# Kernel tuning notes

Hardware: AMD Instinct MI355X
Metric: run time of the kernel (lower is better)

The kernel has to match this reference:

```python
import jax, jax.numpy as jnp
import numpy as np
import math


def setup_inputs() -> dict:
    key = jax.random.key(0)
    ks = jax.random.split(key, 4)
    B, C, H, W, D = 16, 512, 64, 64, 256
    return {
        "x": jax.random.normal(ks[0], (B, C, H, W), jnp.float32),
        "weight_global": jax.random.normal(ks[1], (C, D), jnp.float32) * 0.02,  # trunc_normal std=0.02
        "conv_g_w": jax.random.normal(ks[2], (C, C), jnp.float32) * 0.02,       # 1x1 conv, no bias
        "bn_g_gamma": jnp.ones((C,), jnp.float32),
        "bn_g_beta": jnp.zeros((C,), jnp.float32),
        "conv_c_w": jax.random.normal(ks[3], (C, C), jnp.float32) * 0.02,
        "bn_c_gamma": jnp.ones((C,), jnp.float32),
        "bn_c_beta": jnp.zeros((C,), jnp.float32),
    }


def _bn(x, gamma, beta, eps=1e-5):
    # BatchNorm2d in default training mode: batch statistics over (B, H, W)
    mean = x.mean(axis=(0, 2, 3), keepdims=True)
    var = x.var(axis=(0, 2, 3), keepdims=True)
    xn = (x - mean) * jax.lax.rsqrt(var + eps)
    return xn * gamma[None, :, None, None] + beta[None, :, None, None]


def reference(x, weight_global, conv_g_w, bn_g_gamma, bn_g_beta, conv_c_w, bn_c_gamma, bn_c_beta):
    b, c, h, w = x.shape
    inv_sqrt_c = 1.0 / math.sqrt(c)

    # Description: QR-orthogonal codebook, Q: (c, d)
    Q, _ = jnp.linalg.qr(weight_global + 1e-8)

    # global branch: 1x1 conv -> BN -> ReLU -> global avg pool
    gx = jnp.einsum('oc,bchw->bohw', conv_g_w, x)
    gx = jax.nn.relu(_bn(gx, bn_g_gamma, bn_g_beta))
    g = gx.mean(axis=(2, 3))                                  # (b, c)
    aff_g = jax.nn.softmax((g @ Q) * inv_sqrt_c, axis=1)      # (b, d)
    g = jax.nn.sigmoid(aff_g @ Q.T)                           # (b, c)

    # channel branch: 1x1 conv -> BN -> ReLU
    cx = jnp.einsum('oc,bchw->bohw', conv_c_w, x)
    cx = jax.nn.relu(_bn(cx, bn_c_gamma, bn_c_beta))
    ch = cx.reshape(b, c, h * w).transpose(0, 2, 1)           # (b, hw, c)
    aff_c = jax.nn.softmax((ch @ Q) * inv_sqrt_c, axis=2)     # (b, hw, d)
    # sum(diag_embed(aff_c) @ Q.T, dim=2) == aff_c @ Q.T (fused, avoids (b,hw,d,c) intermediate)
    ch = aff_c @ Q.T                                          # (b, hw, c)

    o = ch * g[:, None, :]
    o = o.transpose(0, 2, 1).reshape(b, c, h, w)
    return o + x
```

## Files before the change

kernel.cpp:

```cpp
#include <hip/hip_runtime.h>
#include <hip/hip_bf16.h>

#define BB 16
#define CC 512
#define HWP 4096
#define DD 256
#define NPIX 65536
#define INV_SQRT_C 0.04419417382415922f

typedef unsigned short u16;
typedef __attribute__((ext_vector_type(8))) short s16x8;
typedef __attribute__((ext_vector_type(8))) unsigned short u16x8;
typedef __attribute__((ext_vector_type(4))) unsigned short u16x4;
typedef __attribute__((ext_vector_type(4))) float f32x4;

__device__ __forceinline__ u16 f2b(float f){
  unsigned int u = __builtin_bit_cast(unsigned int, f);
  unsigned int r = (u + 0x7fffu + ((u >> 16) & 1u)) >> 16;
  return (u16)r;
}

__device__ __forceinline__ f32x4 mfma16(s16x8 a, s16x8 b, f32x4 c){
  return __builtin_amdgcn_mfma_f32_16x16x32_bf16(a, b, c, 0, 0, 0);
}

__global__ __launch_bounds__(256) void k_xbar(const float* __restrict__ x, float* __restrict__ xbar){
  int c = blockIdx.x, tid = threadIdx.x;
  float s = 0.f;
  for (int b = 0; b < BB; ++b){
    const float* px = x + ((size_t)(b*CC + c))*HWP;
    for (int p = tid; p < HWP; p += 256) s += px[p];
  }
  __shared__ float red[256];
  red[tid] = s; __syncthreads();
  for (int st = 128; st; st >>= 1){ if (tid < st) red[tid] += red[tid+st]; __syncthreads(); }
  if (tid == 0) xbar[c] = red[0] * (1.0f/ (float)NPIX);
}

__global__ __launch_bounds__(512) void k_gram(const float* __restrict__ x, float* __restrict__ Spart, int kspl){
  __shared__ __align__(16) u16 Asl[128*72];
  __shared__ __align__(16) u16 Bsl[128*72];
  int tid = threadIdx.x;
  int w = tid >> 6, lane = tid & 63, lr = lane & 15, g = lane >> 4;
  int b = blockIdx.y;
  int kz = blockIdx.z;
  int t = blockIdx.x, ti = 0, rem = 4;
  while (t >= rem){ t -= rem; ++ti; --rem; }
  int tj = ti + t;
  int r0 = ti*128, c0 = tj*128;
  int wm = w >> 2, wn = w & 3;
  f32x4 acc[4][2] = {};
  const float* xb = x + (size_t)b*CC*HWP;
  int klen = HWP / kspl;
  int kbase = kz * klen;
  for (int k0 = kbase; k0 < kbase + klen; k0 += 64){
    __syncthreads();
    for (int tt = tid; tt < 4096; tt += 512){
      int arr = tt >> 11;
      int row = (tt >> 4) & 127;
      int q = tt & 15;
      const float* src = xb + (size_t)((arr ? c0 : r0) + row)*HWP + k0 + q*4;
      f32x4 v = *(const f32x4*)src;
      u16x4 u; u[0]=f2b(v[0]); u[1]=f2b(v[1]); u[2]=f2b(v[2]); u[3]=f2b(v[3]);
      u16* dst = (arr ? Bsl : Asl) + row*72 + q*4;
      *(u16x4*)dst = u;
    }
    __syncthreads();
    #pragma unroll
    for (int kc = 0; kc < 2; ++kc){
      s16x8 av[4], bv[2];
      #pragma unroll
      for (int mt = 0; mt < 4; ++mt) av[mt] = *(const s16x8*)&Asl[(wm*64 + mt*16 + lr)*72 + kc*32 + g*8];
      #pragma unroll
      for (int nt = 0; nt < 2; ++nt) bv[nt] = *(const s16x8*)&Bsl[(wn*32 + nt*16 + lr)*72 + kc*32 + g*8];
      #pragma unroll
      for (int mt = 0; mt < 4; ++mt)
        #pragma unroll
        for (int nt = 0; nt < 2; ++nt)
          acc[mt][nt] = mfma16(av[mt], bv[nt], acc[mt][nt]);
    }
  }
  float* sp = Spart + (size_t)(b*kspl + kz)*262144;
  #pragma unroll
  for (int mt = 0; mt < 4; ++mt)
    #pragma unroll
    for (int nt = 0; nt < 2; ++nt)
      #pragma unroll
      for (int r = 0; r < 4; ++r)
        sp[(size_t)(r0 + wm*64 + mt*16 + 4*g + r)*512 + c0 + wn*32 + nt*16 + lr] = acc[mt][nt][r];
}

__global__ __launch_bounds__(256) void k_sreduce(const float* __restrict__ Spart, float* __restrict__ S, int nslots){
  int idx = blockIdx.x*256 + threadIdx.x;
  int i = idx >> 9, j = idx & 511;
  int src = ((i >> 7) <= (j >> 7)) ? idx : (j*512 + i);
  float s = 0.f;
  for (int k = 0; k < nslots; ++k) s += Spart[(size_t)k*262144 + src];
  S[idx] = s;
}

__global__ __launch_bounds__(256) void k_G(const float* __restrict__ wg, float* __restrict__ G){
  int i = blockIdx.x, j = threadIdx.x;
  float s = 0.f;
  for (int c = 0; c < CC; ++c)
    s = fmaf(wg[c*DD + i] + 1e-8f, wg[c*DD + j] + 1e-8f, s);
  G[i*DD + j] = s;
}

__global__ __launch_bounds__(256) void k_cholPanel(float* __restrict__ G, int kb){
  int tid = threadIdx.x;
  int lane = tid & 63;
  int j = lane & 31;
  int K0 = kb*32;
  float c[32];
  #pragma unroll
  for (int i = 0; i < 32; ++i)
    c[i] = (i <= j) ? G[(K0+i)*DD + K0 + j] : 0.f;
  #pragma unroll
  for (int k = 0; k < 32; ++k){
    float piv = __shfl(c[k], k);
    float sd = sqrtf(piv);
    float ukj = c[k] / sd;
    c[k] = ukj;
    float uk[32];
    #pragma unroll
    for (int i = k + 1; i < 32; ++i) uk[i] = __shfl(ukj, i);
    #pragma unroll
    for (int i = k + 1; i < 32; ++i) c[i] -= uk[i] * ukj;
  }
  if (tid < 32){
    #pragma unroll
    for (int i = 0; i < 32; ++i)
      if (i <= j) G[(K0+i)*DD + K0 + j] = c[i];
  }
  int nt = 256 - K0 - 32;
  int jg = K0 + 32 + tid;
  if (tid < nt){
    float y[32];
    #pragma unroll
    for (int i = 0; i < 32; ++i) y[i] = G[(K0+i)*DD + jg];
    #pragma unroll
    for (int i = 0; i < 32; ++i){
      float s0 = y[i];
      #pragma unroll
      for (int l = 0; l < 32; ++l)
        if (l < i) s0 -= __shfl(c[l], i) * y[l];
      y[i] = s0 / __shfl(c[i], i);
    }
    #pragma unroll
    for (int i = 0; i < 32; ++i) G[(K0+i)*DD + jg] = y[i];
  }
}

__global__ __launch_bounds__(256) void k_cholTrail(float* __restrict__ G, int kb){
  int K0 = kb*32;
  int nt = 256 - K0 - 32;
  int T = (nt + 63) >> 6;
  int t = blockIdx.x, ti = 0, rem = T;
  while (t >= rem){ t -= rem; ++ti; --rem; }
  int tj = ti + t;
  int r0 = K0 + 32 + ti*64;
  int c0 = K0 + 32 + tj*64;
  __shared__ __align__(16) float Ur[32][64];
  __shared__ __align__(16) float Uc[32][64];
  int tid = threadIdx.x;
  for (int idx = tid; idx < 2048; idx += 256){
    int k = idx >> 6, cc = idx & 63;
    int gr = r0 + cc, gc = c0 + cc;
    Ur[k][cc] = (gr < 256) ? G[(K0+k)*DD + gr] : 0.f;
    Uc[k][cc] = (gc < 256) ? G[(K0+k)*DD + gc] : 0.f;
  }
  __syncthreads();
  int tr = (tid >> 4) * 4;
  int tc = (tid & 15) * 4;
  float acc[4][4] = {};
  #pragma unroll
  for (int k = 0; k < 32; ++k){
    f32x4 a = *(const f32x4*)&Ur[k][tr];
    f32x4 b = *(const f32x4*)&Uc[k][tc];
    #pragma unroll
    for (int ii = 0; ii < 4; ++ii)
      #pragma unroll
      for (int jj = 0; jj < 4; ++jj)
        acc[ii][jj] += a[ii]*b[jj];
  }
  #pragma unroll
  for (int ii = 0; ii < 4; ++ii){
    int gi = r0 + tr + ii;
    if (gi >= 256) continue;
    #pragma unroll
    for (int jj = 0; jj < 4; ++jj){
      int gj = c0 + tc + jj;
      if (gj < 256 && gj >= gi)
        G[gi*DD + gj] -= acc[ii][jj];
    }
  }
}

__global__ __launch_bounds__(256) void k_qsolve(const float* __restrict__ G,
    const float* __restrict__ wg,
    float* __restrict__ Q, float* __restrict__ Qst,
    u16* __restrict__ Qb, u16* __restrict__ Qstb){
  __shared__ __align__(16) float Pp[8192];
  __shared__ float Qlds[256*64];
  __shared__ float Wred[3*32*64];
  int tid = threadIdx.x;
  int w = tid >> 6, lane = tid & 63;
  int c = blockIdx.x*64 + lane;
  const float* arow = wg + (size_t)c*DD;

  for (int J = 0; J < 8; ++J){
    int J0 = J*32;
    int nrows8 = (J0 + 32)*8;
    for (int idx = tid; idx < nrows8; idx += 256){
      int row = idx >> 3, q = idx & 7;
      *(f32x4*)&Pp[row*32 + q*4] = *(const f32x4*)&G[row*256 + J0 + q*4];
    }
    __syncthreads();

    float W[32];
    if (w == 0){
      #pragma unroll
      for (int r = 0; r < 32; ++r) W[r] = arow[J0 + r] + 1e-8f;
    } else {
      #pragma unroll
      for (int r = 0; r < 32; ++r) W[r] = 0.f;
    }
    for (int M = w; M < J; M += 4){
      #pragma unroll 4
      for (int k = 0; k < 32; ++k){
        int row = M*32 + k;
        float qv = Qlds[row*64 + lane];
        const float* pr = &Pp[row*32];
        #pragma unroll
        for (int r4 = 0; r4 < 8; ++r4){
          f32x4 p = *(const f32x4*)&pr[r4*4];
          W[r4*4+0] -= qv*p[0];
          W[r4*4+1] -= qv*p[1];
          W[r4*4+2] -= qv*p[2];
          W[r4*4+3] -= qv*p[3];
        }
      }
    }
    if (w > 0){
      #pragma unroll
      for (int r = 0; r < 32; ++r) Wred[((w-1)*32 + r)*64 + lane] = W[r];
    }
    __syncthreads();

    if (w == 0){
      #pragma unroll
      for (int r = 0; r < 32; ++r)
        W[r] += Wred[r*64 + lane] + Wred[(32+r)*64 + lane] + Wred[(64+r)*64 + lane];
      #pragma unroll
      for (int i = 0; i < 32; ++i){
        float t = W[i];
        for (int l = 0; l < i; ++l) t -= W[l] * Pp[(J0 + l)*32 + i];
        W[i] = t / Pp[(J0 + i)*32 + i];
      }
      #pragma unroll
      for (int i = 0; i < 32; ++i) Qlds[(J0 + i)*64 + lane] = W[i];
      #pragma unroll
      for (int r4 = 0; r4 < 8; ++r4){
        f32x4 q4; u16x4 qb4;
        #pragma unroll
        for (int jj = 0; jj < 4; ++jj){ q4[jj] = W[r4*4+jj]; qb4[jj] = f2b(W[r4*4+jj]); }
        *(f32x4*)&Q[(size_t)c*DD + J0 + r4*4] = q4;
        *(u16x4*)&Qb[(size_t)c*DD + J0 + r4*4] = qb4;
      }
      #pragma unroll
      for (int i = 0; i < 32; ++i){
        float qs = W[i] * INV_SQRT_C;
        Qst[(size_t)(J0 + i)*CC + c] = qs;
        Qstb[(size_t)(J0 + i)*CC + c] = f2b(qs);
      }
    }
    __syncthreads();
  }
}

__global__ __launch_bounds__(256) void k_fold(const float* __restrict__ Wg, const float* __restrict__ Wc,
    const float* __restrict__ gamg, const float* __restrict__ betg,
    const float* __restrict__ gamc, const float* __restrict__ betc,
    const float* __restrict__ S, const float* __restrict__ xbar,
    float* __restrict__ Wgf, float* __restrict__ bgf,
    float* __restrict__ Wcf, float* __restrict__ bcf,
    u16* __restrict__ Wgb, u16* __restrict__ Wcb){
  int o = blockIdx.x & 511, br = blockIdx.x >> 9;
  int tid = threadIdx.x;
  const float* W = br ? Wc : Wg;
  __shared__ float wrow[512];
  __shared__ float red[256];
  __shared__ float red2[256];
  __shared__ float sc_s, bi_s;
  wrow[tid] = W[o*512 + tid]; wrow[tid+256] = W[o*512 + tid + 256];
  __syncthreads();
  float mp = 0.f;
  for (int c = tid; c < 512; c += 256) mp = fmaf(wrow[c], xbar[c], mp);
  float qp = 0.f;
  for (int c1 = tid; c1 < 512; c1 += 256){
    const float* srow = S + (size_t)c1*512;
    float y = 0.f;
    for (int c2 = 0; c2 < 512; ++c2) y = fmaf(srow[c2], wrow[c2], y);
    qp = fmaf(wrow[c1], y, qp);
  }
  red[tid] = mp; red2[tid] = qp; __syncthreads();
  for (int st = 128; st; st >>= 1){
    if (tid < st){ red[tid] += red[tid+st]; red2[tid] += red2[tid+st]; }
    __syncthreads();
  }
  if (tid == 0){
    float m = red[0];
    float E = red2[0] * (1.0f/(float)NPIX);
    float var = E - m*m;
    float rstd = rsqrtf(var + 1e-5f);
    float gma = br ? gamc[o] : gamg[o];
    float bta = br ? betc[o] : betg[o];
    sc_s = gma * rstd;
    bi_s = bta - gma * rstd * m;
  }
  __syncthreads();
  float* Wf = br ? Wcf : Wgf;
  float* bf = br ? bcf : bgf;
  u16* Wb  = br ? Wcb : Wgb;
  float w0 = sc_s * wrow[tid], w1 = sc_s * wrow[tid+256];
  Wf[o*512 + tid]     = w0;
  Wf[o*512 + tid+256] = w1;
  Wb[o*512 + tid]     = f2b(w0);
  Wb[o*512 + tid+256] = f2b(w1);
  if (tid == 0) bf[o] = bi_s;
}

__global__ __launch_bounds__(512) void k_gconv(const float* __restrict__ x,
    const u16* __restrict__ Wb, const float* __restrict__ bf, float* __restrict__ gpart){
  __shared__ __align__(16) u16 Xs[64*512];
  int tid = threadIdx.x;
  int w = tid >> 6, lane = tid & 63, lr = lane & 15, g = lane >> 4;
  int slab = blockIdx.x, b = blockIdx.y;
  int p0 = slab*64;

  {
    const float* xb = x + (size_t)b*CC*HWP + p0;
    int p = tid & 63;
    int c8 = (tid >> 6) * 8;
    float v[64];
    #pragma unroll
    for (int pass = 0; pass < 8; ++pass)
      #pragma unroll
      for (int i = 0; i < 8; ++i)
        v[pass*8 + i] = xb[(size_t)(c8 + pass*64 + i)*HWP + p];
    #pragma unroll
    for (int pass = 0; pass < 8; ++pass){
      u16x8 u;
      #pragma unroll
      for (int i = 0; i < 8; ++i) u[i] = f2b(v[pass*8 + i]);
      *(u16x8*)&Xs[p*512 + ((c8 + pass*64) ^ ((p & 7) << 3))] = u;
    }
  }
  __syncthreads();

  f32x4 acc[4][4] = {};
  for (int k = 0; k < 16; ++k){
    int c0 = k*32 + g*8;
    s16x8 bv[4];
    #pragma unroll
    for (int pt = 0; pt < 4; ++pt){
      int p = pt*16 + lr;
      bv[pt] = *(const s16x8*)&Xs[p*512 + (c0 ^ ((p & 7) << 3))];
    }
    #pragma unroll
    for (int i = 0; i < 4; ++i){
      int o0 = (w*4 + i)*16;
      s16x8 a = *(const s16x8*)(Wb + (size_t)(o0 + lr)*512 + c0);
      #pragma unroll
      for (int pt = 0; pt < 4; ++pt)
        acc[i][pt] = mfma16(a, bv[pt], acc[i][pt]);
    }
  }
  #pragma unroll
  for (int i = 0; i < 4; ++i){
    int o0 = (w*4 + i)*16;
    f32x4 bias4 = *(const f32x4*)(bf + o0 + 4*g);
    float s[4] = {0.f, 0.f, 0.f, 0.f};
    #pragma unroll
    for (int pt = 0; pt < 4; ++pt)
      #pragma unroll
      for (int r = 0; r < 4; ++r)
        s[r] += fmaxf(acc[i][pt][r] + bias4[r], 0.f);
    #pragma unroll
    for (int r = 0; r < 4; ++r){
      s[r] += __shfl_xor(s[r], 1);
      s[r] += __shfl_xor(s[r], 2);
      s[r] += __shfl_xor(s[r], 4);
      s[r] += __shfl_xor(s[r], 8);
    }
    if (lr == 0){
      f32x4 sv; sv[0]=s[0]; sv[1]=s[1]; sv[2]=s[2]; sv[3]=s[3];
      *(f32x4*)(gpart + (size_t)(b*64 + slab)*512 + o0 + 4*g) = sv;
    }
  }
}

__global__ __launch_bounds__(256) void k_gvec(const float* __restrict__ gpart, const float* __restrict__ Q,
    const float* __restrict__ Qst, float* __restrict__ gvec){
  int b = blockIdx.x, tid = threadIdx.x;
  __shared__ float g0[512];
  __shared__ float aff[256];
  __shared__ float red[256];
  for (int o = tid; o < 512; o += 256){
    float s = 0.f;
    for (int sl = 0; sl < 64; ++sl) s += gpart[(size_t)(b*64 + sl)*512 + o];
    g0[o] = s * (1.0f/4096.0f);
  }
  __syncthreads();
  float l = 0.f;
  { const float* qr = Qst + (size_t)tid*512;
    for (int c = 0; c < 512; ++c) l = fmaf(qr[c], g0[c], l); }
  red[tid] = l; __syncthreads();
  for (int st = 128; st; st >>= 1){ if (tid < st) red[tid] = fmaxf(red[tid], red[tid+st]); __syncthreads(); }
  float m = red[0]; __syncthreads();
  float e = expf(l - m);
  red[tid] = e; __syncthreads();
  for (int st = 128; st; st >>= 1){ if (tid < st) red[tid] += red[tid+st]; __syncthreads(); }
  float inv = 1.0f/red[0];
  aff[tid] = e * inv;
  __syncthreads();
  for (int o = tid; o < 512; o += 256){
    const float* qr = Q + (size_t)o*DD;
    float v = 0.f;
    for (int d = 0; d < DD; ++d) v = fmaf(aff[d], qr[d], v);
    gvec[b*512 + o] = 1.0f/(1.0f + expf(-v));
  }
}

__global__ __launch_bounds__(512) void k_fused(const float* __restrict__ x,
    const u16* __restrict__ Wcb, const float* __restrict__ bcf,
    const u16* __restrict__ Qstb, const u16* __restrict__ Qb,
    const float* __restrict__ gvec, float* __restrict__ out){
  __shared__ __align__(16) u16 Xs[64*512];
  __shared__ __align__(16) u16 Ts[64*512];
  float* Lsf = (float*)Xs;
  u16*   As  = Ts;
  int tid = threadIdx.x;
  int w = tid >> 6, lane = tid & 63, lr = lane & 15, g = lane >> 4;
  int b = blockIdx.y, p0 = blockIdx.x*64;

  float xr[64];
  {
    const float* xb = x + (size_t)b*CC*HWP + p0;
    int p = tid & 63;
    int c8 = (tid >> 6) * 8;
    float v[64];
    #pragma unroll
    for (int pass = 0; pass < 8; ++pass)
      #pragma unroll
      for (int i = 0; i < 8; ++i)
        v[pass*8 + i] = xb[(size_t)(c8 + pass*64 + i)*HWP + p];
    #pragma unroll
    for (int pass = 0; pass < 8; ++pass){
      u16x8 u;
      #pragma unroll
      for (int i = 0; i < 8; ++i) u[i] = f2b(v[pass*8 + i]);
      *(u16x8*)&Xs[p*512 + ((c8 + pass*64) ^ ((p & 7) << 3))] = u;
    }
    #pragma unroll
    for (int i = 0; i < 4; ++i)
      #pragma unroll
      for (int pt = 0; pt < 4; ++pt)
        #pragma unroll
        for (int r = 0; r < 4; ++r)
          xr[(i*4 + pt)*4 + r] =
            x[(size_t)(b*CC + (w*4 + i)*16 + 4*g + r)*HWP + p0 + pt*16 + lr];
  }
  __syncthreads();

  {
    f32x4 acc[4][4] = {};
    for (int k = 0; k < 16; ++k){
      int c0 = k*32 + g*8;
      s16x8 bv[4];
      #pragma unroll
      for (int pt = 0; pt < 4; ++pt){
        int p = pt*16 + lr;
        bv[pt] = *(const s16x8*)&Xs[p*512 + (c0 ^ ((p & 7) << 3))];
      }
      #pragma unroll
      for (int i = 0; i < 4; ++i){
        int o0 = (w*4 + i)*16;
        s16x8 a = *(const s16x8*)(Wcb + (size_t)(o0 + lr)*512 + c0);
        #pragma unroll
        for (int pt = 0; pt < 4; ++pt)
          acc[i][pt] = mfma16(a, bv[pt], acc[i][pt]);
      }
    }
    #pragma unroll
    for (int i = 0; i < 4; ++i){
      int o0 = (w*4 + i)*16;
      f32x4 bias4 = *(const f32x4*)(bcf + o0 + 4*g);
      #pragma unroll
      for (int pt = 0; pt < 4; ++pt){
        int p = pt*16 + lr;
        u16x4 u;
        #pragma unroll
        for (int r = 0; r < 4; ++r) u[r] = f2b(fmaxf(acc[i][pt][r] + bias4[r], 0.f));
        *(u16x4*)&Ts[p*512 + ((o0 + 4*g) ^ ((p & 7) << 3))] = u;
      }
    }
  }
  __syncthreads();

  {
    f32x4 acc[2][4] = {};
    for (int k = 0; k < 16; ++k){
      int o0 = k*32 + g*8;
      s16x8 bv[4];
      #pragma unroll
      for (int pt = 0; pt < 4; ++pt){
        int p = pt*16 + lr;
        bv[pt] = *(const s16x8*)&Ts[p*512 + (o0 ^ ((p & 7) << 3))];
      }
      #pragma unroll
      for (int i = 0; i < 2; ++i){
        int d0 = (w*2 + i)*16;
        s16x8 a = *(const s16x8*)(Qstb + (size_t)(d0 + lr)*512 + o0);
        #pragma unroll
        for (int pt = 0; pt < 4; ++pt)
          acc[i][pt] = mfma16(a, bv[pt], acc[i][pt]);
      }
    }
    #pragma unroll
    for (int i = 0; i < 2; ++i){
      int d0 = (w*2 + i)*16;
      #pragma unroll
      for (int pt = 0; pt < 4; ++pt){
        int p = pt*16 + lr;
        *(f32x4*)&Lsf[p*256 + ((d0 + 4*g) ^ ((p & 7) << 2))] = acc[i][pt];
      }
    }
  }
  __syncthreads();

  {
    int px = tid >> 3, sub = tid & 7;
    float* Lrow = Lsf + px*256;
    int sw2 = (px & 7) << 2, sw3 = (px & 7) << 3;
    float v[32];
    #pragma unroll
    for (int jj = 0; jj < 8; ++jj){
      int d0 = sub*32 + jj*4;
      f32x4 t = *(const f32x4*)&Lrow[d0 ^ sw2];
      v[jj*4+0] = t[0]; v[jj*4+1] = t[1]; v[jj*4+2] = t[2]; v[jj*4+3] = t[3];
    }
    float m = v[0];
    #pragma unroll
    for (int jj = 1; jj < 32; ++jj) m = fmaxf(m, v[jj]);
    m = fmaxf(m, __shfl_xor(m, 1));
    m = fmaxf(m, __shfl_xor(m, 2));
    m = fmaxf(m, __shfl_xor(m, 4));
    float s = 0.f;
    #pragma unroll
    for (int jj = 0; jj < 32; ++jj){ v[jj] = __expf(v[jj] - m); s += v[jj]; }
    s += __shfl_xor(s, 1);
    s += __shfl_xor(s, 2);
    s += __shfl_xor(s, 4);
    float inv = 1.0f/s;
    #pragma unroll
    for (int jj = 0; jj < 4; ++jj){
      int d0 = sub*32 + jj*8;
      u16x8 u;
      #pragma unroll
      for (int i = 0; i < 8; ++i) u[i] = f2b(v[jj*8+i] * inv);
      *(u16x8*)&As[px*256 + (d0 ^ sw3)] = u;
    }
  }
  __syncthreads();

  {
    f32x4 acc[4][4] = {};
    for (int k = 0; k < 8; ++k){
      int d0 = k*32 + g*8;
      s16x8 bv[4];
      #pragma unroll
      for (int pt = 0; pt < 4; ++pt){
        int p = pt*16 + lr;
        bv[pt] = *(const s16x8*)&As[p*256 + (d0 ^ ((p & 7) << 3))];
      }
      #pragma unroll
      for (int i = 0; i < 4; ++i){
        int o0 = (w*4 + i)*16;
        s16x8 a = *(const s16x8*)(Qb + (size_t)(o0 + lr)*256 + d0);
        #pragma unroll
        for (int pt = 0; pt < 4; ++pt)
          acc[i][pt] = mfma16(a, bv[pt], acc[i][pt]);
      }
    }
    #pragma unroll
    for (int i = 0; i < 4; ++i){
      int o0 = (w*4 + i)*16;
      f32x4 gg = *(const f32x4*)(gvec + b*512 + o0 + 4*g);
      #pragma unroll
      for (int pt = 0; pt < 4; ++pt){
        #pragma unroll
        for (int r = 0; r < 4; ++r){
          size_t idx = (size_t)(b*CC + o0 + 4*g + r)*HWP + p0 + pt*16 + lr;
          out[idx] = fmaf(acc[i][pt][r], gg[r], xr[(i*4 + pt)*4 + r]);
        }
      }
    }
  }
}

extern "C" void kernel_launch(void* const* d_in, const int* in_sizes, int n_in,
                              void* d_out, int out_size, void* d_ws, size_t ws_size,
                              hipStream_t stream) {
  const float* x    = (const float*)d_in[0];
  const float* wg   = (const float*)d_in[1];
  const float* Wg   = (const float*)d_in[2];
  const float* gamg = (const float*)d_in[3];
  const float* betg = (const float*)d_in[4];
  const float* Wc   = (const float*)d_in[5];
  const float* gamc = (const float*)d_in[6];
  const float* betc = (const float*)d_in[7];
  float* out = (float*)d_out;

  int kspl = 1;
  {
    size_t need2 = ((size_t)1320448 + 2*16*262144 + 524288 + 393216) * 4;
    if (ws_size >= need2) kspl = 2;
  }

  float* ws = (float*)d_ws;
  float* G     = ws + 0;
  float* Q     = ws + 131072;
  float* Qst   = ws + 262144;
  float* S     = ws + 393216;
  float* xbar  = ws + 655360;
  float* Wgf   = ws + 655872;
  float* bgf   = ws + 918016;
  float* Wcf   = ws + 918528;
  float* bcf   = ws + 1180672;
  float* gvec  = ws + 1181184;
  float* Spart = ws + 1320448;
  float* gpart = Spart + (size_t)kspl*16*262144;
  u16*   ub    = (u16*)(gpart + 524288);
  u16* Qb   = ub;
  u16* Qstb = ub + 131072;
  u16* Wgb  = ub + 262144;
  u16* Wcb  = ub + 524288;

  k_xbar<<<512, 256, 0, stream>>>(x, xbar);
  k_gram<<<dim3(10,16,kspl), 512, 0, stream>>>(x, Spart, kspl);
  k_sreduce<<<1024, 256, 0, stream>>>(Spart, S, 16*kspl);
  k_G<<<256, 256, 0, stream>>>(wg, G);
  for (int kb = 0; kb < 8; ++kb){
    k_cholPanel<<<1, 256, 0, stream>>>(G, kb);
    int nt = 256 - kb*32 - 32;
    if (nt > 0){
      int T = (nt + 63) >> 6;
      k_cholTrail<<<T*(T+1)/2, 256, 0, stream>>>(G, kb);
    }
  }
  k_qsolve<<<8, 256, 0, stream>>>(G, wg, Q, Qst, Qb, Qstb);
  k_fold<<<1024, 256, 0, stream>>>(Wg, Wc, gamg, betg, gamc, betc, S, xbar, Wgf, bgf, Wcf, bcf, Wgb, Wcb);
  k_gconv<<<dim3(64,16), 512, 0, stream>>>(x, Wgb, bgf, gpart);
  k_gvec<<<16, 256, 0, stream>>>(gpart, Q, Qst, gvec);
  k_fused<<<dim3(64,16), 512, 0, stream>>>(x, Wcb, bcf, Qstb, Qb, gvec, out);
}
```

Measured before the change: 946.7 us.

## Fuse channel-mean computation into Gram kernel and coalesce fold kernel quadratic form

Removes the separate k_xbar pass over x by accumulating per-channel sums inside the diagonal-tile blocks of the Gram kernel while they load x anyway, combining them with atomics into a memset buffer. Separately, k_fold's S·w product is restructured so each wavefront handles one S row, with lanes reading contiguous elements and a shuffle reduction, instead of each thread walking a whole row serially. This saves one full 128MB read of x and improves memory coalescing in the fold, at the cost of atomics and nondeterministic summation order.

```diff
diff --git a/kernel.cpp b/kernel.cpp
--- a/kernel.cpp
+++ b/kernel.cpp
@@ -24,20 +24,8 @@
   return __builtin_amdgcn_mfma_f32_16x16x32_bf16(a, b, c, 0, 0, 0);
 }
 
-__global__ __launch_bounds__(256) void k_xbar(const float* __restrict__ x, float* __restrict__ xbar){
-  int c = blockIdx.x, tid = threadIdx.x;
-  float s = 0.f;
-  for (int b = 0; b < BB; ++b){
-    const float* px = x + ((size_t)(b*CC + c))*HWP;
-    for (int p = tid; p < HWP; p += 256) s += px[p];
-  }
-  __shared__ float red[256];
-  red[tid] = s; __syncthreads();
-  for (int st = 128; st; st >>= 1){ if (tid < st) red[tid] += red[tid+st]; __syncthreads(); }
-  if (tid == 0) xbar[c] = red[0] * (1.0f/ (float)NPIX);
-}
-
-__global__ __launch_bounds__(512) void k_gram(const float* __restrict__ x, float* __restrict__ Spart, int kspl){
+__global__ __launch_bounds__(512) void k_gram(const float* __restrict__ x, float* __restrict__ Spart,
+                                              float* __restrict__ xbar, int kspl){
   __shared__ __align__(16) u16 Asl[128*72];
   __shared__ __align__(16) u16 Bsl[128*72];
   int tid = threadIdx.x;
@@ -48,19 +36,24 @@
   while (t >= rem){ t -= rem; ++ti; --rem; }
   int tj = ti + t;
   int r0 = ti*128, c0 = tj*128;
+  bool isdiag = (ti == tj);
   int wm = w >> 2, wn = w & 3;
   f32x4 acc[4][2] = {};
+  float xsum[8] = {};
   const float* xb = x + (size_t)b*CC*HWP;
   int klen = HWP / kspl;
   int kbase = kz * klen;
   for (int k0 = kbase; k0 < kbase + klen; k0 += 64){
     __syncthreads();
-    for (int tt = tid; tt < 4096; tt += 512){
+    #pragma unroll
+    for (int s = 0; s < 8; ++s){
+      int tt = tid + s*512;
       int arr = tt >> 11;
       int row = (tt >> 4) & 127;
       int q = tt & 15;
       const float* src = xb + (size_t)((arr ? c0 : r0) + row)*HWP + k0 + q*4;
       f32x4 v = *(const f32x4*)src;
+      if (isdiag && arr == 0) xsum[s] += (v[0]+v[1]) + (v[2]+v[3]);
       u16x4 u; u[0]=f2b(v[0]); u[1]=f2b(v[1]); u[2]=f2b(v[2]); u[3]=f2b(v[3]);
       u16* dst = (arr ? Bsl : Asl) + row*72 + q*4;
       *(u16x4*)dst = u;
@@ -88,6 +81,26 @@
       #pragma unroll
       for (int r = 0; r < 4; ++r)
         sp[(size_t)(r0 + wm*64 + mt*16 + 4*g + r)*512 + c0 + wn*32 + nt*16 + lr] = acc[mt][nt][r];
+
+  if (isdiag){
+    __syncthreads();
+    float* scr = (float*)Asl;
+    #pragma unroll
+    for (int s = 0; s < 8; ++s){
+      int tt = tid + s*512;
+      if ((tt >> 11) == 0){
+        int row = (tt >> 4) & 127, q = tt & 15;
+        scr[row*16 + q] = xsum[s];
+      }
+    }
+    __syncthreads();
+    if (tid < 128){
+      float rs = 0.f;
+      #pragma unroll
+      for (int j = 0; j < 16; ++j) rs += scr[tid*16 + j];
+      atomicAdd(&xbar[r0 + tid], rs * (1.0f/(float)NPIX));
+    }
+  }
 }
 
 __global__ __launch_bounds__(256) void k_sreduce(const float* __restrict__ Spart, float* __restrict__ S, int nslots){
@@ -288,30 +301,44 @@
     u16* __restrict__ Wgb, u16* __restrict__ Wcb){
   int o = blockIdx.x & 511, br = blockIdx.x >> 9;
   int tid = threadIdx.x;
+  int wv = tid >> 6, lane = tid & 63;
   const float* W = br ? Wc : Wg;
   __shared__ float wrow[512];
   __shared__ float red[256];
-  __shared__ float red2[256];
+  __shared__ float yred[4];
   __shared__ float sc_s, bi_s;
   wrow[tid] = W[o*512 + tid]; wrow[tid+256] = W[o*512 + tid + 256];
   __syncthreads();
+
+  float qp = 0.f;
+  for (int c1 = wv; c1 < 512; c1 += 4){
+    const float* srow = S + (size_t)c1*512;
+    float y = 0.f;
+    #pragma unroll
+    for (int c8 = 0; c8 < 8; ++c8){
+      int c2 = lane + c8*64;
+      y = fmaf(srow[c2], wrow[c2], y);
+    }
+    y += __shfl_xor(y, 1);
+    y += __shfl_xor(y, 2);
+    y += __shfl_xor(y, 4);
+    y += __shfl_xor(y, 8);
+    y += __shfl_xor(y, 16);
+    y += __shfl_xor(y, 32);
+    qp = fmaf(wrow[c1], y, qp);
+  }
+  if (lane == 0) yred[wv] = qp;
+
   float mp = 0.f;
   for (int c = tid; c < 512; c += 256) mp = fmaf(wrow[c], xbar[c], mp);
-  float qp = 0.f;
-  for (int c1 = tid; c1 < 512; c1 += 256){
-    const float* srow = S + (size_t)c1*512;
-    float y = 0.f;
-    for (int c2 = 0; c2 < 512; ++c2) y = fmaf(srow[c2], wrow[c2], y);
-    qp = fmaf(wrow[c1], y, qp);
-  }
-  red[tid] = mp; red2[tid] = qp; __syncthreads();
+  red[tid] = mp; __syncthreads();
   for (int st = 128; st; st >>= 1){
-    if (tid < st){ red[tid] += red[tid+st]; red2[tid] += red2[tid+st]; }
+    if (tid < st) red[tid] += red[tid+st];
     __syncthreads();
   }
   if (tid == 0){
     float m = red[0];
-    float E = red2[0] * (1.0f/(float)NPIX);
+    float E = (yred[0] + yred[1] + yred[2] + yred[3]) * (1.0f/(float)NPIX);
     float var = E - m*m;
     float rstd = rsqrtf(var + 1e-5f);
     float gma = br ? gamc[o] : gamg[o];
@@ -648,8 +675,8 @@
   u16* Wgb  = ub + 262144;
   u16* Wcb  = ub + 524288;
 
-  k_xbar<<<512, 256, 0, stream>>>(x, xbar);
-  k_gram<<<dim3(10,16,kspl), 512, 0, stream>>>(x, Spart, kspl);
+  hipMemsetAsync(xbar, 0, 512*sizeof(float), stream);
+  k_gram<<<dim3(10,16,kspl), 512, 0, stream>>>(x, Spart, xbar, kspl);
   k_sreduce<<<1024, 256, 0, stream>>>(Spart, S, 16*kspl);
   k_G<<<256, 256, 0, stream>>>(wg, G);
   for (int kb = 0; kb < 8; ++kb){
```

New measurement: 826.7 us. 1.15x faster.
